# Performance work log

Hardware: AMD Instinct MI355X
Metric: run time of the kernel (lower is better)

## Reference

```python
import jax, jax.numpy as jnp
import numpy as np

B, N, D, M, L = 64, 4096, 128, 1024, 128  # batch, set size, d_in, num_ref_points, num_projections


def setup_inputs() -> dict:
    key = jax.random.key(0)
    k1, k2, k3, k4 = jax.random.split(key, 4)
    X = jax.random.normal(k1, (B, N, D), dtype=jnp.float32)
    theta_v = jax.random.normal(k2, (L, D), dtype=jnp.float32)          # weight_norm 'v' param
    ref_points = jax.random.normal(k3, (M, L), dtype=jnp.float32)       # self.reference
    weight = jax.random.normal(k4, (L, M), dtype=jnp.float32) * 0.04    # xavier-ish self.weight
    return {"X": X, "theta_v": theta_v, "ref_points": ref_points, "weight": weight}


def reference(X, theta_v, ref_points, weight):
    # weight_norm(dim=0) with g fixed to 1: effective row-normalized projection matrix
    W = theta_v / jnp.linalg.norm(theta_v, axis=1, keepdims=True)       # [L, D]
    slices = jnp.einsum('bnd,ld->bnl', X, W)                            # [B, N, L]
    s = jnp.sort(slices, axis=1)                                        # sort each slice over the set dim

    # M != N: linear interp of sorted values onto the M-point grid (torchinterp1d equivalent;
    # xnew range is strictly inside x range since M < N, so clamping never triggers)
    x = jnp.linspace(0.0, 1.0, N + 2)[1:-1]                             # [N]
    xnew = jnp.linspace(0.0, 1.0, M + 2)[1:-1]                          # [M]
    y = jnp.transpose(s, (0, 2, 1)).reshape(B * L, N)                   # [B*L, N]
    interp = jax.vmap(lambda yr: jnp.interp(xnew, x, yr))(y)            # [B*L, M]
    interp = jnp.transpose(interp.reshape(B, L, M), (0, 2, 1))          # [B, M, L]

    # gather interpolated quantiles by the sort order of the reference set
    Rind = jnp.argsort(ref_points, axis=0)                              # [M, L]
    gathered = jnp.take_along_axis(interp, jnp.broadcast_to(Rind[None], (B, M, L)), axis=1)
    diff = ref_points[None, :, :] - gathered                            # [B, M, L]

    # weighted sum over reference points per projection
    return jnp.einsum('bml,lm->bl', diff, weight)                       # [B, L]
```

## Files before the change

### kernel.cpp

```cpp
#include <hip/hip_runtime.h>

static constexpr int Bc = 64;
static constexpr int Nc = 4096;
static constexpr int Dc = 128;
static constexpr int Mc = 1024;
static constexpr int Lc = 128;

using short8   = __attribute__((ext_vector_type(8))) short;
using ushort8v = __attribute__((ext_vector_type(8))) unsigned short;
using f32x4    = __attribute__((ext_vector_type(4))) float;

__device__ __forceinline__ unsigned short f2bf(float x) {
  unsigned u = __builtin_bit_cast(unsigned, x);
  return (unsigned short)((u + 0x7FFFu + ((u >> 16) & 1u)) >> 16);
}
__device__ __forceinline__ float bf2f(unsigned short h) {
  unsigned u = ((unsigned)h) << 16;
  return __builtin_bit_cast(float, u);
}

__device__ __forceinline__ int swz(int i) { return i ^ ((i >> 4) & 31); }

__global__ __launch_bounds__(256) void setup_kernel(
    const float* __restrict__ theta_v, const float* __restrict__ ref,
    const float* __restrict__ weight, unsigned short* __restrict__ Wh,
    unsigned short* __restrict__ Wl, float* __restrict__ C,
    float* __restrict__ v) {
  constexpr int NBv = 2048;
  constexpr float LOv = -4.2f;
  constexpr float SCv = (float)NBv / 8.4f;

  __shared__ int pref[NBv];
  __shared__ float skey[Mc];
  __shared__ unsigned short sidx[Mc];
  __shared__ float vrow[Nc];
  __shared__ int wsum[4];
  __shared__ float s2[2];
  __shared__ float c4[4];

  int l = blockIdx.x;
  int tid = threadIdx.x;
  int lane = tid & 63, wv = tid >> 6;

  float x[4];
  #pragma unroll
  for (int j = 0; j < 4; ++j) x[j] = ref[(size_t)(tid + 256 * j) * Lc + l];

  for (int i = tid; i < NBv; i += 256) pref[i] = 0;
  for (int i = tid; i < Nc; i += 256) vrow[i] = 0.f;

  float wval = 0.f;
  if (tid < Dc) {
    wval = theta_v[l * Dc + tid];
    float sq = wval * wval;
    #pragma unroll
    for (int off = 1; off < 64; off <<= 1) sq += __shfl_xor(sq, off, 64);
    if (lane == 0) s2[wv] = sq;
  }
  {
    float cacc = 0.f;
    #pragma unroll
    for (int j = 0; j < 4; ++j) cacc += x[j] * weight[(size_t)l * Mc + tid + 256 * j];
    #pragma unroll
    for (int off = 1; off < 64; off <<= 1) cacc += __shfl_xor(cacc, off, 64);
    if (lane == 0) c4[wv] = cacc;
  }
  __syncthreads();

  if (tid < Dc) {
    float norm = sqrtf(s2[0] + s2[1]);
    float val = wval / norm;
    unsigned short hi = f2bf(val);
    Wh[l * Dc + tid] = hi;
    Wl[l * Dc + tid] = f2bf(val - bf2f(hi));
  }
  if (tid == 0) C[l] = c4[0] + c4[1] + c4[2] + c4[3];

  int bb[4];
  #pragma unroll
  for (int j = 0; j < 4; ++j) {
    int bi = (int)((x[j] - LOv) * SCv);
    bi = bi < 0 ? 0 : (bi > NBv - 1 ? NBv - 1 : bi);
    bb[j] = bi;
    atomicAdd(&pref[swz(bi)], 1);
  }
  __syncthreads();

  {
    int base_ = tid * 8;
    int loc[8]; int s = 0;
    #pragma unroll
    for (int j = 0; j < 8; ++j) loc[j] = pref[swz(base_ + j)];
    #pragma unroll
    for (int j = 0; j < 8; ++j) { int c = loc[j]; loc[j] = s; s += c; }
    int inc = s;
    #pragma unroll
    for (int off = 1; off < 64; off <<= 1) {
      int o = __shfl_up(inc, off, 64);
      if (lane >= off) inc += o;
    }
    if (lane == 63) wsum[wv] = inc;
    __syncthreads();
    int wbase = 0;
    #pragma unroll
    for (int ww = 0; ww < 4; ++ww) if (ww < wv) wbase += wsum[ww];
    int tbase = wbase + inc - s;
    #pragma unroll
    for (int j = 0; j < 8; ++j) pref[swz(base_ + j)] = tbase + loc[j];
  }
  __syncthreads();

  #pragma unroll
  for (int j = 0; j < 4; ++j) {
    int p = atomicAdd(&pref[swz(bb[j])], 1);
    skey[p] = x[j];
    sidx[p] = (unsigned short)(tid + 256 * j);
  }
  __syncthreads();

  #pragma unroll
  for (int k = 0; k < 4; ++k) {
    int p = tid + 256 * k;
    float y = skey[p];
    int m = sidx[p];
    int b = (int)((y - LOv) * SCv);
    b = b < 0 ? 0 : (b > NBv - 1 ? NBv - 1 : b);
    int lo_ = b ? pref[swz(b - 1)] : 0;
    int hi_ = pref[swz(b)];
    int r = lo_;
    for (int q = lo_; q < hi_; ++q) {
      float z = skey[q];
      r += (z < y || (z == y && sidx[q] < m)) ? 1 : 0;
    }
    float wvv = weight[(size_t)l * Mc + r];
    double pos = (double)(m + 1) * (double)(Nc + 1) / (double)(Mc + 1) - 1.0;
    int i0 = (int)pos;
    float t = (float)(pos - (double)i0);
    atomicAdd(&vrow[i0], (1.0f - t) * wvv);
    atomicAdd(&vrow[i0 + 1], t * wvv);
  }
  __syncthreads();
  for (int i = tid; i < Nc; i += 256) v[(size_t)l * Nc + i] = vrow[i];
}

__global__ __launch_bounds__(512) void gemm_kernel(
    const float* __restrict__ X, const unsigned short* __restrict__ Whp,
    const unsigned short* __restrict__ Wlp, float* __restrict__ sl) {
  __shared__ unsigned short Bh[2][128][40];
  __shared__ unsigned short Bl[2][128][40];

  int bloc = blockIdx.y;
  int nbase = blockIdx.x * 128;
  int tid = threadIdx.x;
  int lane = tid & 63;
  int wv = tid >> 6;
  int m16 = lane & 15;
  int kg = lane >> 4;

  int brow = tid >> 2;
  int bc = (tid & 3) * 8;
  const unsigned short* gbh = Whp + (size_t)brow * Dc + bc;
  const unsigned short* gbl = Wlp + (size_t)brow * Dc + bc;

  const float* arow = X + ((size_t)bloc * Nc + nbase + wv * 16 + m16) * Dc + kg * 8;
  float4 af[4][2];
  #pragma unroll
  for (int c = 0; c < 4; ++c) {
    af[c][0] = *(const float4*)(arow + c * 32);
    af[c][1] = *(const float4*)(arow + c * 32 + 4);
  }

  ushort8v rbh = *(const ushort8v*)gbh;
  ushort8v rbl = *(const ushort8v*)gbl;
  *(ushort8v*)&Bh[0][brow][bc] = rbh;
  *(ushort8v*)&Bl[0][brow][bc] = rbl;
  rbh = *(const ushort8v*)(gbh + 32);
  rbl = *(const ushort8v*)(gbl + 32);

  f32x4 acc[8] = {};
  __syncthreads();

  #pragma unroll
  for (int c = 0; c < 4; ++c) {
    if (c < 3) {
      *(ushort8v*)&Bh[(c + 1) & 1][brow][bc] = rbh;
      *(ushort8v*)&Bl[(c + 1) & 1][brow][bc] = rbl;
    }
    if (c < 2) {
      rbh = *(const ushort8v*)(gbh + (c + 2) * 32);
      rbl = *(const ushort8v*)(gbl + (c + 2) * 32);
    }

    float xs[8] = {af[c][0].x, af[c][0].y, af[c][0].z, af[c][0].w,
                   af[c][1].x, af[c][1].y, af[c][1].z, af[c][1].w};
    short8 ah, al;
    #pragma unroll
    for (int e = 0; e < 8; ++e) {
      unsigned short h = f2bf(xs[e]);
      ah[e] = (short)h;
      al[e] = (short)f2bf(xs[e] - bf2f(h));
    }

    #pragma unroll
    for (int u = 0; u < 8; ++u) {
      short8 bh = *(const short8*)&Bh[c & 1][u * 16 + m16][kg * 8];
      short8 bl = *(const short8*)&Bl[c & 1][u * 16 + m16][kg * 8];
      acc[u] = __builtin_amdgcn_mfma_f32_16x16x32_bf16(ah, bh, acc[u], 0, 0, 0);
      acc[u] = __builtin_amdgcn_mfma_f32_16x16x32_bf16(ah, bl, acc[u], 0, 0, 0);
      acc[u] = __builtin_amdgcn_mfma_f32_16x16x32_bf16(al, bh, acc[u], 0, 0, 0);
    }
    __syncthreads();
  }

  #pragma unroll
  for (int u = 0; u < 8; ++u) {
    int l = u * 16 + m16;
    int n0 = nbase + wv * 16 + kg * 4;
    float* dst = sl + ((size_t)bloc * Lc + l) * Nc + n0;
    *(float4*)dst = *(float4*)&acc[u];
  }
}

__device__ __forceinline__ int gbin(float x) {
  constexpr int NB = 4096;
  float t = __builtin_amdgcn_exp2f(x * -2.45541f);
  float r = __builtin_amdgcn_rcpf(1.0f + t);
  int bi = (int)((float)NB * r);
  return bi < 0 ? 0 : (bi > NB - 1 ? NB - 1 : bi);
}

__global__ __launch_bounds__(512, 8) void rank_dot_kernel(
    const float* __restrict__ sl, const float* __restrict__ v,
    const float* __restrict__ C, float* __restrict__ out, int b0) {
  constexpr int NB = 4096;
  constexpr int NT = 512;
  constexpr int EL = Nc / NT;

  __shared__ int pref[NB];
  __shared__ __align__(16) float skey[Nc];
  int* wsum = (int*)skey;
  float* red = (float*)pref;

  int l = blockIdx.x & (Lc - 1);
  int bloc = blockIdx.x >> 7;
  int tid = threadIdx.x;
  const float* src = sl + ((size_t)bloc * Lc + l) * Nc;

  float x[EL];
  {
    const float4* s4 = (const float4*)src;
    #pragma unroll
    for (int j = 0; j < EL / 4; ++j) {
      float4 f = s4[tid + NT * j];
      x[j * 4 + 0] = f.x; x[j * 4 + 1] = f.y;
      x[j * 4 + 2] = f.z; x[j * 4 + 3] = f.w;
    }
  }

  for (int i = tid; i < NB; i += NT) pref[i] = 0;
  __syncthreads();

  int bb[EL];
  int ofs[EL];
  #pragma unroll
  for (int j = 0; j < EL; ++j) {
    int bi = gbin(x[j]);
    bb[j] = bi;
    ofs[j] = atomicAdd(&pref[swz(bi)], 1);
  }
  __syncthreads();

  {
    int base_ = tid * 8;
    int loc[8]; int s = 0;
    #pragma unroll
    for (int j = 0; j < 8; ++j) loc[j] = pref[swz(base_ + j)];
    #pragma unroll
    for (int j = 0; j < 8; ++j) { int c = loc[j]; loc[j] = s; s += c; }
    int lane = tid & 63, wvv = tid >> 6;
    int inc = s;
    #pragma unroll
    for (int off = 1; off < 64; off <<= 1) {
      int o = __shfl_up(inc, off, 64);
      if (lane >= off) inc += o;
    }
    if (lane == 63) wsum[wvv] = inc;
    __syncthreads();
    int wbase = 0;
    #pragma unroll
    for (int ww = 0; ww < 8; ++ww) if (ww < wvv) wbase += wsum[ww];
    int tbase = wbase + inc - s;
    #pragma unroll
    for (int j = 0; j < 8; ++j) pref[swz(base_ + j)] = tbase + loc[j];
  }
  __syncthreads();

  #pragma unroll
  for (int j = 0; j < EL; ++j) {
    skey[pref[swz(bb[j])] + ofs[j]] = x[j];
  }
  __syncthreads();

  const f32x4* skey4 = (const f32x4*)skey;
  const float* vrow = v + (size_t)l * Nc;
  float acc = 0.f;
  #pragma unroll
  for (int k = 0; k < EL; ++k) {
    int p = tid + NT * k;
    float y = skey[p];
    int b = gbin(y);
    int lo_ = pref[swz(b)];
    int hi_ = (b == NB - 1) ? Nc : pref[swz(b + 1)];
    int q4 = lo_ >> 2;
    int e4 = (hi_ + 3) >> 2;
    int r = q4 << 2;
    for (; q4 < e4; ++q4) {
      f32x4 z = skey4[q4];
      int qb = q4 << 2;
      r += (z[0] < y || (z[0] == y && qb + 0 < p)) ? 1 : 0;
      r += (z[1] < y || (z[1] == y && qb + 1 < p)) ? 1 : 0;
      r += (z[2] < y || (z[2] == y && qb + 2 < p)) ? 1 : 0;
      r += (z[3] < y || (z[3] == y && qb + 3 < p)) ? 1 : 0;
    }
    acc += y * vrow[r];
  }

  #pragma unroll
  for (int off = 1; off < 64; off <<= 1) acc += __shfl_xor(acc, off, 64);
  __syncthreads();
  if ((tid & 63) == 0) red[tid >> 6] = acc;
  __syncthreads();
  if (tid == 0) {
    float t = 0.f;
    #pragma unroll
    for (int ww = 0; ww < 8; ++ww) t += red[ww];
    int b = b0 + bloc;
    out[(size_t)b * Lc + l] = C[l] - t;
  }
}

extern "C" void kernel_launch(void* const* d_in, const int* in_sizes, int n_in,
                              void* d_out, int out_size, void* d_ws, size_t ws_size,
                              hipStream_t stream) {
  const float* X       = (const float*)d_in[0];
  const float* theta_v = (const float*)d_in[1];
  const float* ref     = (const float*)d_in[2];
  const float* weight  = (const float*)d_in[3];
  float* out = (float*)d_out;

  float* v  = (float*)d_ws;
  unsigned short* Wh = (unsigned short*)(v + (size_t)Lc * Nc);
  unsigned short* Wl = Wh + (size_t)Lc * Dc;
  float* Cc = (float*)(Wl + (size_t)Lc * Dc);
  float* sl = Cc + 128;
  size_t used = (size_t)((char*)sl - (char*)d_ws);
  size_t per_b = (size_t)Lc * Nc * sizeof(float);
  int chunk = 1;
  if (ws_size > used + per_b) {
    size_t c = (ws_size - used) / per_b;
    chunk = (int)(c > (size_t)Bc ? (size_t)Bc : c);
    if (chunk < 1) chunk = 1;
  }

  setup_kernel<<<Lc, 256, 0, stream>>>(theta_v, ref, weight, Wh, Wl, Cc, v);

  for (int b0 = 0; b0 < Bc; b0 += chunk) {
    int nb = (Bc - b0) < chunk ? (Bc - b0) : chunk;
    dim3 g1(Nc / 128, nb);
    gemm_kernel<<<g1, 512, 0, stream>>>(X + (size_t)b0 * Nc * Dc, Wh, Wl, sl);
    rank_dot_kernel<<<(size_t)nb * Lc, 512, 0, stream>>>(sl, v, Cc, out, b0);
  }
}
```

Baseline: 151.9 us.

## Store projected slices as bf16 and rank on packed bin/key integers

The GEMM now writes the projected slices as bf16 instead of fp32, halving the intermediate buffer written by the GEMM and read back by the rank kernel. The rank kernel loads 8 bf16 values per thread and maps each to an order-preserving 16-bit integer. It packs the histogram bin into the upper 16 bits, so rank comparisons become integer compares and the second gbin evaluation is dropped. Rounding slices to bf16 adds quantisation error and more ties, which could push the output past tolerance.

```diff
diff --git a/kernel.cpp b/kernel.cpp
--- a/kernel.cpp
+++ b/kernel.cpp
@@ -9,6 +9,7 @@
 using short8   = __attribute__((ext_vector_type(8))) short;
 using ushort8v = __attribute__((ext_vector_type(8))) unsigned short;
 using f32x4    = __attribute__((ext_vector_type(4))) float;
+using u32x4    = __attribute__((ext_vector_type(4))) unsigned;
 
 __device__ __forceinline__ unsigned short f2bf(float x) {
   unsigned u = __builtin_bit_cast(unsigned, x);
@@ -145,7 +146,7 @@
 
 __global__ __launch_bounds__(512) void gemm_kernel(
     const float* __restrict__ X, const unsigned short* __restrict__ Whp,
-    const unsigned short* __restrict__ Wlp, float* __restrict__ sl) {
+    const unsigned short* __restrict__ Wlp, unsigned short* __restrict__ sl) {
   __shared__ unsigned short Bh[2][128][40];
   __shared__ unsigned short Bl[2][128][40];
 
@@ -216,8 +217,11 @@
   for (int u = 0; u < 8; ++u) {
     int l = u * 16 + m16;
     int n0 = nbase + wv * 16 + kg * 4;
-    float* dst = sl + ((size_t)bloc * Lc + l) * Nc + n0;
-    *(float4*)dst = *(float4*)&acc[u];
+    unsigned short* dst = sl + ((size_t)bloc * Lc + l) * Nc + n0;
+    ushort4 o;
+    o.x = f2bf(acc[u][0]); o.y = f2bf(acc[u][1]);
+    o.z = f2bf(acc[u][2]); o.w = f2bf(acc[u][3]);
+    *(ushort4*)dst = o;
   }
 }
 
@@ -230,34 +234,37 @@
 }
 
 __global__ __launch_bounds__(512, 8) void rank_dot_kernel(
-    const float* __restrict__ sl, const float* __restrict__ v,
+    const unsigned short* __restrict__ sl, const float* __restrict__ v,
     const float* __restrict__ C, float* __restrict__ out, int b0) {
   constexpr int NB = 4096;
   constexpr int NT = 512;
   constexpr int EL = Nc / NT;
 
   __shared__ int pref[NB];
-  __shared__ __align__(16) float skey[Nc];
-  int* wsum = (int*)skey;
+  __shared__ __align__(16) unsigned cell[Nc];
+  int* wsum = (int*)cell;
   float* red = (float*)pref;
 
   int l = blockIdx.x & (Lc - 1);
   int bloc = blockIdx.x >> 7;
   int tid = threadIdx.x;
-  const float* src = sl + ((size_t)bloc * Lc + l) * Nc;
-
+  const unsigned short* src = sl + ((size_t)bloc * Lc + l) * Nc;
+
+  ushort8v kv = *(const ushort8v*)(src + (size_t)tid * 8);
   float x[EL];
+  unsigned mk[EL];
+  #pragma unroll
+  for (int j = 0; j < EL; ++j) {
+    unsigned short u = (unsigned short)kv[j];
+    x[j] = bf2f(u);
+    mk[j] = (u & 0x8000u) ? (unsigned)(u ^ 0xFFFFu) : (unsigned)(u | 0x8000u);
+  }
+
   {
-    const float4* s4 = (const float4*)src;
-    #pragma unroll
-    for (int j = 0; j < EL / 4; ++j) {
-      float4 f = s4[tid + NT * j];
-      x[j * 4 + 0] = f.x; x[j * 4 + 1] = f.y;
-      x[j * 4 + 2] = f.z; x[j * 4 + 3] = f.w;
-    }
-  }
-
-  for (int i = tid; i < NB; i += NT) pref[i] = 0;
+    int4 z = make_int4(0, 0, 0, 0);
+    ((int4*)pref)[tid] = z;
+    ((int4*)pref)[tid + NT] = z;
+  }
   __syncthreads();
 
   int bb[EL];
@@ -297,32 +304,36 @@
 
   #pragma unroll
   for (int j = 0; j < EL; ++j) {
-    skey[pref[swz(bb[j])] + ofs[j]] = x[j];
-  }
-  __syncthreads();
-
-  const f32x4* skey4 = (const f32x4*)skey;
+    int pos = pref[swz(bb[j])] + ofs[j];
+    cell[pos] = ((unsigned)bb[j] << 16) | mk[j];
+  }
+  __syncthreads();
+
+  const u32x4* cell4 = (const u32x4*)cell;
   const float* vrow = v + (size_t)l * Nc;
   float acc = 0.f;
   #pragma unroll
   for (int k = 0; k < EL; ++k) {
     int p = tid + NT * k;
-    float y = skey[p];
-    int b = gbin(y);
+    unsigned yc = cell[p];
+    int b = (int)(yc >> 16);
     int lo_ = pref[swz(b)];
     int hi_ = (b == NB - 1) ? Nc : pref[swz(b + 1)];
     int q4 = lo_ >> 2;
     int e4 = (hi_ + 3) >> 2;
     int r = q4 << 2;
     for (; q4 < e4; ++q4) {
-      f32x4 z = skey4[q4];
+      u32x4 z = cell4[q4];
       int qb = q4 << 2;
-      r += (z[0] < y || (z[0] == y && qb + 0 < p)) ? 1 : 0;
-      r += (z[1] < y || (z[1] == y && qb + 1 < p)) ? 1 : 0;
-      r += (z[2] < y || (z[2] == y && qb + 2 < p)) ? 1 : 0;
-      r += (z[3] < y || (z[3] == y && qb + 3 < p)) ? 1 : 0;
-    }
-    acc += y * vrow[r];
+      r += (z[0] < yc || (z[0] == yc && qb + 0 < p)) ? 1 : 0;
+      r += (z[1] < yc || (z[1] == yc && qb + 1 < p)) ? 1 : 0;
+      r += (z[2] < yc || (z[2] == yc && qb + 2 < p)) ? 1 : 0;
+      r += (z[3] < yc || (z[3] == yc && qb + 3 < p)) ? 1 : 0;
+    }
+    unsigned short k16 = (unsigned short)(yc & 0xFFFFu);
+    unsigned short ub = (k16 & 0x8000u) ? (unsigned short)(k16 ^ 0x8000u)
+                                        : (unsigned short)(k16 ^ 0xFFFFu);
+    acc += bf2f(ub) * vrow[r];
   }
 
   #pragma unroll
@@ -352,9 +363,9 @@
   unsigned short* Wh = (unsigned short*)(v + (size_t)Lc * Nc);
   unsigned short* Wl = Wh + (size_t)Lc * Dc;
   float* Cc = (float*)(Wl + (size_t)Lc * Dc);
-  float* sl = Cc + 128;
+  unsigned short* sl = (unsigned short*)(Cc + 128);
   size_t used = (size_t)((char*)sl - (char*)d_ws);
-  size_t per_b = (size_t)Lc * Nc * sizeof(float);
+  size_t per_b = (size_t)Lc * Nc * sizeof(unsigned short);
   int chunk = 1;
   if (ws_size > used + per_b) {
     size_t c = (ws_size - used) / per_b;
```

New measurement: 158.8 us (median of 2 runs). 1.05x slower.
